# Performance work log

Hardware: AMD Instinct MI355X
Metric: run time of the kernel (lower is better)

The kernel has to match this reference:

```python
import jax, jax.numpy as jnp
import numpy as np

DIM, DIM_K, DIM_U, HEADS, SCOPE = 256, 16, 1, 4, 23
DIM_V = DIM // HEADS  # 64
EPS = 1e-5


def _bn(x, gamma, beta):
    # training-mode BatchNorm2d over (b, h, w), biased variance, per-channel affine
    mean = jnp.mean(x, axis=(0, 2, 3), keepdims=True)
    var = jnp.var(x, axis=(0, 2, 3), keepdims=True)
    xhat = (x - mean) * jax.lax.rsqrt(var + EPS)
    return xhat * gamma[None, :, None, None] + beta[None, :, None, None]


def setup_inputs() -> dict:
    key = jax.random.key(0)
    ks = jax.random.split(key, 8)
    c_out = HEADS * DIM_K + DIM_K * DIM_U + DIM_V * DIM_U  # 144
    x = jax.random.normal(ks[0], (16, DIM, 64, 64), dtype=jnp.float32)
    w_qkv = jax.random.normal(ks[1], (c_out, DIM), dtype=jnp.float32) * (1.0 / np.sqrt(DIM))
    gamma_q = jnp.ones((HEADS * DIM_K,), jnp.float32)
    beta_q = jnp.zeros((HEADS * DIM_K,), jnp.float32)
    gamma_v = jnp.ones((DIM_V * DIM_U,), jnp.float32)
    beta_v = jnp.zeros((DIM_V * DIM_U,), jnp.float32)
    fan_in = DIM_U * SCOPE * SCOPE
    w_lconv = jax.random.normal(ks[2], (DIM_K, DIM_U, 1, SCOPE, SCOPE), dtype=jnp.float32) * (1.0 / np.sqrt(fan_in))
    b_lconv = jnp.zeros((DIM_K,), jnp.float32)
    return {"x": x, "w_qkv": w_qkv, "gamma_q": gamma_q, "beta_q": beta_q,
            "gamma_v": gamma_v, "beta_v": beta_v, "w_lconv": w_lconv, "b_lconv": b_lconv}


def reference(x, w_qkv, gamma_q, beta_q, gamma_v, beta_v, w_lconv, b_lconv):
    b, c, h, w = x.shape
    m = h * w
    # 1x1 conv projection
    qkv = jnp.einsum('oc,bchw->bohw', w_qkv, x)
    q = qkv[:, :HEADS * DIM_K]
    k = qkv[:, HEADS * DIM_K:HEADS * DIM_K + DIM_K * DIM_U]
    v = qkv[:, HEADS * DIM_K + DIM_K * DIM_U:]
    # q: 'b (k n) h w -> b n k m'
    q = _bn(q, gamma_q, beta_q).reshape(b, DIM_K, HEADS, m).transpose(0, 2, 1, 3)
    # v: 'b (v u) h w -> b u v m'
    v = _bn(v, gamma_v, beta_v).reshape(b, DIM_V, DIM_U, m).transpose(0, 2, 1, 3)
    # k: 'b (u k) h w -> b u k m', softmax over m
    k = jax.nn.softmax(k.reshape(b, DIM_U, DIM_K, m), axis=-1)
    content_lambda = jnp.einsum('bukm,buvm->bkv', k, v)
    # position lambda: Conv3d over (v, h, w) with kernel (1, scope, scope)
    v5 = v.reshape(b, DIM_U, DIM_V, h, w)
    pad = (SCOPE - 1) // 2
    pl = jax.lax.conv_general_dilated(
        v5, w_lconv, window_strides=(1, 1, 1),
        padding=[(0, 0), (pad, pad), (pad, pad)],
        dimension_numbers=('NCDHW', 'OIDHW', 'NCDHW'))
    pl = pl + b_lconv[None, :, None, None, None]
    position_lambda = pl.reshape(b, DIM_K, DIM_V, m)
    content_output = jnp.einsum('bnkm,bkv->bnvm', q, content_lambda)
    position_output = jnp.einsum('bnkm,bkvm->bnvm', q, position_lambda)
    out = (content_output + position_output).reshape(b, HEADS * DIM_V, h, w)
    return out
```

## Files before the change

kernel.cpp:

```cpp
#include <hip/hip_runtime.h>
#include <math.h>

#define NB    16
#define CDIM  256
#define COUT  144
#define MPIX  4096
#define SCOPE 23
#define PADH  11
#define BNEPS 1e-5f

typedef __attribute__((ext_vector_type(4))) float f32x4;
typedef __attribute__((ext_vector_type(8))) short s16x8;

__device__ __forceinline__ unsigned short f2bf(float f) {
    unsigned u = __builtin_bit_cast(unsigned, f);
    unsigned r = (u + 0x7FFFu + ((u >> 16) & 1u)) >> 16;
    return (unsigned short)r;
}

__global__ void prep_frags(const float* __restrict__ w, const float* __restrict__ wl,
                           short* __restrict__ wqf, short* __restrict__ wfrag) {
    int i = blockIdx.x * 256 + threadIdx.x;
    if (i < 36864) {
        int j = i & 7, lane = (i >> 3) & 63;
        int fi = i >> 9;
        int mf = fi % 9, kc = fi / 9;
        int o = mf * 16 + (lane & 15);
        int c = kc * 32 + (lane >> 4) * 8 + j;
        wqf[i] = (short)f2bf(w[o * 256 + c]);
        return;
    }
    int i2 = i - 36864;
    if (i2 < 23 * 64 * 8) {
        int j = i2 & 7, l = (i2 >> 3) & 63, dy = i2 >> 9;
        int k = l & 15, t = ((l >> 4) << 3) + j;
        float wv = (t < SCOPE) ? wl[k * 529 + dy * 23 + t] : 0.f;
        wfrag[i2] = (short)f2bf(wv);
    }
}

__global__ void __launch_bounds__(256, 4) gemm_qkv(const float* __restrict__ x,
                                                   const short* __restrict__ wqf,
                                                   float* __restrict__ qkv) {
    __shared__ unsigned pk[16 * 65];
    int mt = blockIdx.x, b = blockIdx.y;
    int m0 = mt * 64;
    int tid = threadIdx.x;
    int px64 = tid & 63, c2b = tid >> 6;
    int lane = tid & 63, wv = tid >> 6;
    int pxl = lane & 15, kgq = lane >> 4;
    const float* xb = x + (size_t)b * CDIM * MPIX;
    float* qtb = qkv + (size_t)b * COUT * MPIX;
    const s16x8* wfv = (const s16x8*)wqf;

    f32x4 acc[9];
#pragma unroll
    for (int mf = 0; mf < 9; mf++) acc[mf] = 0.f;

#pragma unroll 1
    for (int kc = 0; kc < 8; kc++) {
        if (kc > 0) __syncthreads();
#pragma unroll
        for (int it = 0; it < 4; it++) {
            int c2 = c2b + it * 4;
            float x0 = xb[(size_t)(kc * 32 + 2 * c2) * MPIX + m0 + px64];
            float x1 = xb[(size_t)(kc * 32 + 2 * c2 + 1) * MPIX + m0 + px64];
            pk[c2 * 65 + px64] = (unsigned)f2bf(x0) | ((unsigned)f2bf(x1) << 16);
        }
        __syncthreads();
        const unsigned* bp = &pk[kgq * 4 * 65 + wv * 16 + pxl];
        int4 bi = make_int4(bp[0], bp[65], bp[130], bp[195]);
        s16x8 bf = __builtin_bit_cast(s16x8, bi);
#pragma unroll
        for (int mf = 0; mf < 9; mf++) {
            s16x8 af = wfv[(kc * 9 + mf) * 64 + lane];
            acc[mf] = __builtin_amdgcn_mfma_f32_16x16x32_bf16(af, bf, acc[mf], 0, 0, 0);
        }
    }

    int m = m0 + wv * 16 + pxl;
#pragma unroll
    for (int mf = 0; mf < 9; mf++) {
#pragma unroll
        for (int r = 0; r < 4; r++) {
            int o = mf * 16 + kgq * 4 + r;
            if (mf < 4) qtb[(size_t)m * 64 + o] = acc[mf][r];
            else qkv[((size_t)b * COUT + o) * MPIX + m] = acc[mf][r];
        }
    }
}

__global__ void stats_q(const float* __restrict__ qkv, float* __restrict__ qpart) {
    int mc = blockIdx.x, b = blockIdx.y;
    const float* qb = qkv + (size_t)b * COUT * MPIX;
    int tid = threadIdx.x;
    int c = tid & 63, mg = tid >> 6;
    float s = 0.f, s2 = 0.f;
#pragma unroll 4
    for (int i = 0; i < 64; i++) {
        int m = mc * 256 + i * 4 + mg;
        float v = qb[(size_t)m * 64 + c];
        s += v;
        s2 = fmaf(v, v, s2);
    }
    __shared__ float rs[4][64], rs2[4][64];
    rs[mg][c] = s;
    rs2[mg][c] = s2;
    __syncthreads();
    if (tid < 64) {
        float ts = rs[0][tid] + rs[1][tid] + rs[2][tid] + rs[3][tid];
        float ts2 = rs2[0][tid] + rs2[1][tid] + rs2[2][tid] + rs2[3][tid];
        qpart[(((size_t)tid * 16 + b) * 16 + mc) * 2 + 0] = ts;
        qpart[(((size_t)tid * 16 + b) * 16 + mc) * 2 + 1] = ts2;
    }
}

__global__ void stats_v(const float* __restrict__ qkv, float* __restrict__ part) {
    int cx = blockIdx.x, b = blockIdx.y;
    const float* row = qkv + ((size_t)b * COUT + 80 + cx) * MPIX;
    int tid = threadIdx.x;
    float s = 0.f, s2 = 0.f;
    for (int i = tid; i < MPIX; i += 256) {
        float v = row[i];
        s += v;
        s2 = fmaf(v, v, s2);
    }
#pragma unroll
    for (int off = 32; off > 0; off >>= 1) {
        s += __shfl_down(s, off);
        s2 += __shfl_down(s2, off);
    }
    __shared__ float red[8];
    int wid = tid >> 6, lane = tid & 63;
    if (lane == 0) { red[wid * 2] = s; red[wid * 2 + 1] = s2; }
    __syncthreads();
    if (tid == 0) {
        float ts = 0.f, ts2 = 0.f;
#pragma unroll
        for (int w2 = 0; w2 < 4; w2++) { ts += red[w2 * 2]; ts2 += red[w2 * 2 + 1]; }
        part[(size_t)((64 + cx) * 16 + b) * 2 + 0] = ts;
        part[(size_t)((64 + cx) * 16 + b) * 2 + 1] = ts2;
    }
}

__global__ void stats_finalize(const float* __restrict__ part,
                               const float* __restrict__ qpart,
                               const float* __restrict__ gq, const float* __restrict__ bq,
                               const float* __restrict__ gv, const float* __restrict__ bv,
                               float* __restrict__ ascale, float* __restrict__ dshift) {
    int ch = threadIdx.x;
    if (ch >= 128) return;
    float s = 0.f, s2 = 0.f;
    if (ch < 64) {
        for (int i = 0; i < 256; i++) {
            s += qpart[((size_t)ch * 256 + i) * 2 + 0];
            s2 += qpart[((size_t)ch * 256 + i) * 2 + 1];
        }
    } else {
        for (int b = 0; b < 16; b++) {
            s += part[(size_t)(ch * 16 + b) * 2 + 0];
            s2 += part[(size_t)(ch * 16 + b) * 2 + 1];
        }
    }
    const float invN = 1.0f / 65536.0f;
    float mean = s * invN;
    float var = s2 * invN - mean * mean;
    float g = (ch < 64) ? gq[ch] : gv[ch - 64];
    float be = (ch < 64) ? bq[ch] : bv[ch - 64];
    float a = g * rsqrtf(var + BNEPS);
    ascale[ch] = a;
    dshift[ch] = be - mean * a;
}

__global__ void softmax_k(const float* __restrict__ qkv, float* __restrict__ p) {
    int bk = blockIdx.x;
    int b = bk >> 4, kc = bk & 15;
    const float* row = qkv + ((size_t)b * COUT + 64 + kc) * MPIX;
    int tid = threadIdx.x;
    float v[16];
    float mx = -INFINITY;
#pragma unroll
    for (int i = 0; i < 16; i++) {
        v[i] = row[tid + i * 256];
        mx = fmaxf(mx, v[i]);
    }
#pragma unroll
    for (int off = 32; off > 0; off >>= 1) mx = fmaxf(mx, __shfl_down(mx, off));
    __shared__ float redm[4];
    __shared__ float bm;
    int wid = tid >> 6, lane = tid & 63;
    if (lane == 0) redm[wid] = mx;
    __syncthreads();
    if (tid == 0) bm = fmaxf(fmaxf(redm[0], redm[1]), fmaxf(redm[2], redm[3]));
    __syncthreads();
    mx = bm;
    float s = 0.f;
#pragma unroll
    for (int i = 0; i < 16; i++) {
        v[i] = expf(v[i] - mx);
        s += v[i];
    }
#pragma unroll
    for (int off = 32; off > 0; off >>= 1) s += __shfl_down(s, off);
    __shared__ float reds[4];
    __shared__ float bs;
    if (lane == 0) reds[wid] = s;
    __syncthreads();
    if (tid == 0) bs = reds[0] + reds[1] + reds[2] + reds[3];
    __syncthreads();
    float r = 1.0f / bs;
    float* prow = p + ((size_t)b * 16 + kc) * MPIX;
#pragma unroll
    for (int i = 0; i < 16; i++) prow[tid + i * 256] = v[i] * r;
}

__global__ void cl_partial(const float* __restrict__ qkv, const float* __restrict__ p,
                           const float* __restrict__ ascale, const float* __restrict__ dshift,
                           float* __restrict__ clpart) {
    __shared__ float vsT[128][65];
    int mc = blockIdx.x, b = blockIdx.y;
    int m0 = mc * 256;
    int tid = threadIdx.x;
    int vc = tid & 63, kg = tid >> 6;
    float acc[4] = {0.f, 0.f, 0.f, 0.f};
    for (int half = 0; half < 2; half++) {
        int mh = m0 + half * 128;
        __syncthreads();
        for (int i = tid; i < 64 * 128; i += 256) {
            int r = i >> 7, c = i & 127;
            vsT[c][r] = fmaf(ascale[64 + r], qkv[((size_t)b * COUT + 80 + r) * MPIX + mh + c],
                             dshift[64 + r]);
        }
        __syncthreads();
        for (int mm = 0; mm < 128; mm++) {
            float vv = vsT[mm][vc];
#pragma unroll
            for (int i = 0; i < 4; i++) {
                int kc = kg * 4 + i;
                acc[i] = fmaf(p[((size_t)b * 16 + kc) * MPIX + mh + mm], vv, acc[i]);
            }
        }
    }
#pragma unroll
    for (int i = 0; i < 4; i++) {
        int kc = kg * 4 + i;
        clpart[(((size_t)b * 16 + mc) * 16 + kc) * 64 + vc] = acc[i];
    }
}

__global__ void cl_reduce(const float* __restrict__ clpart, float* __restrict__ cl) {
    int b = blockIdx.x;
    for (int o = threadIdx.x; o < 1024; o += 256) {
        float s = 0.f;
        for (int mc = 0; mc < 16; mc++)
            s += clpart[((size_t)b * 16 + mc) * 1024 + o];
        cl[(size_t)b * 1024 + o] = s;
    }
}

__global__ void __launch_bounds__(256) bnq_t(float* __restrict__ qkv,
                                             const float* __restrict__ ascale,
                                             const float* __restrict__ dshift) {
    __shared__ float sv[64][65];
    int mt = blockIdx.x, b = blockIdx.y;
    int m0 = mt * 64;
    float* qb = qkv + (size_t)b * COUT * MPIX;
    int tid = threadIdx.x;
    int c = tid & 63, mg = tid >> 6;
    float a = ascale[c], d = dshift[c];
#pragma unroll
    for (int i = 0; i < 16; i++) {
        int m = mg * 16 + i;
        sv[m][c] = fmaf(a, qb[(size_t)(m0 + m) * 64 + c], d);
    }
    __syncthreads();
    int m = tid >> 2, jb = (tid & 3) * 8;
    unsigned dw[8];
#pragma unroll
    for (int j = 0; j < 8; j++) {
        int cc = jb * 2 + 2 * j;
        dw[j] = (unsigned)f2bf(sv[m][cc]) | ((unsigned)f2bf(sv[m][cc + 1]) << 16);
    }
    unsigned* dst = (unsigned*)qb + (size_t)(m0 + m) * 64 + jb;
    *(uint4*)dst = make_uint4(dw[0], dw[1], dw[2], dw[3]);
    *(uint4*)(dst + 4) = make_uint4(dw[4], dw[5], dw[6], dw[7]);
}

#define SPW 88
#define LD_FRAG(P) __builtin_bit_cast(s16x8, make_int4((P)[0], (P)[2], (P)[4], (P)[6]))
#define STEP(DY, J) do {                                                        \
    const unsigned* pnew_ = xbase + ((DY) + 3) * SPW;                           \
    rw[((J) + 3) & 3][0] = LD_FRAG(pnew_);                                      \
    rw[((J) + 3) & 3][1] = LD_FRAG(pnew_ + 16);                                 \
    int dyn_ = ((DY) + 3 < 22) ? (DY) + 3 : 22;                                 \
    wr[((J) + 3) & 3] = wf[dyn_ * 64 + lane];                                   \
    _Pragma("unroll")                                                           \
    for (int ty_ = 0; ty_ < 4; ty_++) {                                         \
      _Pragma("unroll")                                                         \
      for (int x2_ = 0; x2_ < 2; x2_++) {                                       \
        int t_ = ty_ * 2 + x2_;                                                 \
        acc[t_] = __builtin_amdgcn_mfma_f32_16x16x32_bf16(                      \
            wr[(J) & 3], rw[((J) + ty_) & 3][x2_], acc[t_], 0, 0, 0);           \
      }                                                                         \
    }                                                                           \
  } while (0)

__global__ void __launch_bounds__(256, 4) lambda_main(
    const float* __restrict__ qkv, const float* __restrict__ ascale,
    const float* __restrict__ dshift, const float* __restrict__ cl,
    const short* __restrict__ wfrag, const float* __restrict__ bl,
    float* __restrict__ out) {
    __shared__ unsigned spack[54 * SPW + 8];
    __shared__ float sck[16];

    int vc = blockIdx.x, b = blockIdx.y, h = blockIdx.z;
    int tid = threadIdx.x;

    if (tid < 16) sck[tid] = cl[((size_t)b * 16 + tid) * 64 + vc] + bl[tid];

    float av = ascale[64 + vc], dv = dshift[64 + vc];
    const float* vrow = qkv + ((size_t)b * COUT + 80 + vc) * MPIX;
    for (int i = tid; i < 54 * SPW; i += 256) {
        int y = i / SPW, e = i - y * SPW;
        int iy = h * 32 + y - PADH;
        float f0 = 0.f, f1 = 0.f;
        if ((unsigned)iy < 64u) {
            int ix0 = e - PADH, ix1 = e - PADH + 1;
            if ((unsigned)ix0 < 64u) f0 = fmaf(av, vrow[iy * 64 + ix0], dv);
            if ((unsigned)ix1 < 64u) f1 = fmaf(av, vrow[iy * 64 + ix1], dv);
        }
        spack[i] = (unsigned)f2bf(f0) | ((unsigned)f2bf(f1) << 16);
    }
    if (tid < 8) spack[54 * SPW + tid] = 0u;
    __syncthreads();

    int lane = tid & 63;
    int wv = tid >> 6;
    int px = lane & 15;
    int kg = lane >> 4;
    const s16x8* wf = (const s16x8*)wfrag;

    const unsigned* qtb = (const unsigned*)(qkv + (size_t)b * COUT * MPIX);
    float* ob = out + (size_t)b * 256 * MPIX;

    float sck_l[4];
#pragma unroll
    for (int r = 0; r < 4; r++) sck_l[r] = sck[kg * 4 + r];

#pragma unroll 1
    for (int gg = 0; gg < 2; gg++) {
        int y0 = (gg * 4 + wv) * 4;
        const unsigned* base = &spack[y0 * SPW + px + kg * 8];

#pragma unroll 1
        for (int xh = 0; xh < 2; xh++) {
            const unsigned* xbase = base + xh * 32;
            f32x4 acc[8];
#pragma unroll
            for (int t = 0; t < 8; t++) acc[t] = 0.f;

            s16x8 rw[4][2];
            s16x8 wr[4];
#pragma unroll
            for (int r0 = 0; r0 < 3; r0++) {
                const unsigned* p = xbase + r0 * SPW;
                rw[r0][0] = LD_FRAG(p);
                rw[r0][1] = LD_FRAG(p + 16);
            }
#pragma unroll
            for (int s = 0; s < 3; s++) wr[s] = wf[s * 64 + lane];

#pragma unroll 1
            for (int i8 = 0; i8 < 2; i8++) {
                int dyb = i8 * 8;
                STEP(dyb + 0, 0);
                STEP(dyb + 1, 1);
                STEP(dyb + 2, 2);
                STEP(dyb + 3, 3);
                STEP(dyb + 4, 4);
                STEP(dyb + 5, 5);
                STEP(dyb + 6, 6);
                STEP(dyb + 7, 7);
            }
            STEP(16, 0);
            STEP(17, 1);
            STEP(18, 2);
            STEP(19, 3);
            STEP(20, 4);
            STEP(21, 5);
            STEP(22, 6);

#pragma unroll
            for (int t = 0; t < 8; t++) {
                int ty = t >> 1, x2 = t & 1;
                int m0 = (h * 32 + y0 + ty) * 64 + (xh * 2 + x2) * 16;
                float lam[4];
#pragma unroll
                for (int r = 0; r < 4; r++) lam[r] = acc[t][r] + sck_l[r];
                const unsigned* qp = &qtb[(size_t)(m0 + px) * 64 + kg * 8];
                uint4 qa = *(const uint4*)qp;
                uint4 qb4 = *(const uint4*)(qp + 4);
                unsigned dws[8] = {qa.x, qa.y, qa.z, qa.w, qb4.x, qb4.y, qb4.z, qb4.w};
                float po[4] = {0.f, 0.f, 0.f, 0.f};
#pragma unroll
                for (int d = 0; d < 8; d++) {
                    float q0 = __builtin_bit_cast(float, dws[d] << 16);
                    float q1 = __builtin_bit_cast(float, dws[d] & 0xffff0000u);
                    int i0 = 2 * d, i1 = 2 * d + 1;
                    po[i0 & 3] = fmaf(q0, lam[i0 >> 2], po[i0 & 3]);
                    po[i1 & 3] = fmaf(q1, lam[i1 >> 2], po[i1 & 3]);
                }
#pragma unroll
                for (int n = 0; n < 4; n++) {
                    po[n] += __shfl_xor(po[n], 16);
                    po[n] += __shfl_xor(po[n], 32);
                }
                float sv = (kg == 0) ? po[0] : (kg == 1) ? po[1] : (kg == 2) ? po[2] : po[3];
                ob[(size_t)(kg * 64 + vc) * MPIX + m0 + px] = sv;
            }
        }
    }
}

extern "C" void kernel_launch(void* const* d_in, const int* in_sizes, int n_in,
                              void* d_out, int out_size, void* d_ws, size_t ws_size,
                              hipStream_t stream) {
    const float* x      = (const float*)d_in[0];
    const float* w_qkv  = (const float*)d_in[1];
    const float* gq     = (const float*)d_in[2];
    const float* bq     = (const float*)d_in[3];
    const float* gv     = (const float*)d_in[4];
    const float* bv     = (const float*)d_in[5];
    const float* wl     = (const float*)d_in[6];
    const float* bl     = (const float*)d_in[7];
    float* out = (float*)d_out;

    float* ws     = (float*)d_ws;
    float* qkv    = ws;
    float* p      = qkv + 9437184;
    float* part   = p + 1048576;
    float* ascale = part + 4096;
    float* dshift = ascale + 128;
    float* clpart = dshift + 128;
    float* clb    = clpart + 262144;
    short* wfrag  = (short*)(clb + 16384);
    short* wqf    = (short*)(clb + 16384 + 5888 + 64);
    float* qpart  = (float*)(wqf + 36864);

    prep_frags<<<190, 256, 0, stream>>>(w_qkv, wl, wqf, wfrag);
    gemm_qkv<<<dim3(64, 16), 256, 0, stream>>>(x, wqf, qkv);
    stats_q<<<dim3(16, 16), 256, 0, stream>>>(qkv, qpart);
    stats_v<<<dim3(64, 16), 256, 0, stream>>>(qkv, part);
    stats_finalize<<<1, 128, 0, stream>>>(part, qpart, gq, bq, gv, bv, ascale, dshift);
    softmax_k<<<256, 256, 0, stream>>>(qkv, p);
    cl_partial<<<dim3(16, 16), 256, 0, stream>>>(qkv, p, ascale, dshift, clpart);
    cl_reduce<<<16, 256, 0, stream>>>(clpart, clb);
    bnq_t<<<dim3(64, 16), 256, 0, stream>>>(qkv, ascale, dshift);
    lambda_main<<<dim3(64, 16, 2), 256, 0, stream>>>(qkv, ascale, dshift, clb, wfrag, bl, out);
}
```

Baseline: 208.7 us.

## Fuse BatchNorm channel statistics into QKV GEMM epilogue

Computes per-channel sum and sum-of-squares of the projection output inside the GEMM epilogue, using lane shuffles and a shared-memory reduction across waves. This replaces the separate stats_q and stats_v kernels, which reread the q and v regions of the qkv buffer from global memory. The finalize kernel becomes a 128-block parallel reduction over 1024 partials per channel. In exchange the GEMM gains extra shuffles, shared memory and a barrier, which may reduce its occupancy, and it also computes statistics for the unused k channels.

```diff
diff --git a/kernel.cpp b/kernel.cpp
--- a/kernel.cpp
+++ b/kernel.cpp
@@ -41,8 +41,10 @@
 
 __global__ void __launch_bounds__(256, 4) gemm_qkv(const float* __restrict__ x,
                                                    const short* __restrict__ wqf,
-                                                   float* __restrict__ qkv) {
+                                                   float* __restrict__ qkv,
+                                                   float* __restrict__ statpart) {
     __shared__ unsigned pk[16 * 65];
+    __shared__ float ssum[4][144], ssq[4][144];
     int mt = blockIdx.x, b = blockIdx.y;
     int m0 = mt * 64;
     int tid = threadIdx.x;
@@ -88,42 +90,47 @@
             else qkv[((size_t)b * COUT + o) * MPIX + m] = acc[mf][r];
         }
     }
-}
-
-__global__ void stats_q(const float* __restrict__ qkv, float* __restrict__ qpart) {
-    int mc = blockIdx.x, b = blockIdx.y;
-    const float* qb = qkv + (size_t)b * COUT * MPIX;
-    int tid = threadIdx.x;
-    int c = tid & 63, mg = tid >> 6;
+
+#pragma unroll
+    for (int mf = 0; mf < 9; mf++) {
+#pragma unroll
+        for (int r = 0; r < 4; r++) {
+            float s = acc[mf][r];
+            float s2 = s * s;
+#pragma unroll
+            for (int off = 1; off < 16; off <<= 1) {
+                s += __shfl_xor(s, off);
+                s2 += __shfl_xor(s2, off);
+            }
+            if (pxl == 0) {
+                int ch = mf * 16 + kgq * 4 + r;
+                ssum[wv][ch] = s;
+                ssq[wv][ch] = s2;
+            }
+        }
+    }
+    __syncthreads();
+    if (tid < 144) {
+        float s = ssum[0][tid] + ssum[1][tid] + ssum[2][tid] + ssum[3][tid];
+        float s2 = ssq[0][tid] + ssq[1][tid] + ssq[2][tid] + ssq[3][tid];
+        size_t idx = (((size_t)tid * 16 + b) * 64 + mt) * 2;
+        statpart[idx + 0] = s;
+        statpart[idx + 1] = s2;
+    }
+}
+
+__global__ void stats_finalize(const float* __restrict__ statpart,
+                               const float* __restrict__ gq, const float* __restrict__ bq,
+                               const float* __restrict__ gv, const float* __restrict__ bv,
+                               float* __restrict__ ascale, float* __restrict__ dshift) {
+    int sch = blockIdx.x;
+    int gch = (sch < 64) ? sch : sch + 16;
+    const float* sp = statpart + (size_t)gch * 1024 * 2;
+    int tid = threadIdx.x;
     float s = 0.f, s2 = 0.f;
-#pragma unroll 4
-    for (int i = 0; i < 64; i++) {
-        int m = mc * 256 + i * 4 + mg;
-        float v = qb[(size_t)m * 64 + c];
-        s += v;
-        s2 = fmaf(v, v, s2);
-    }
-    __shared__ float rs[4][64], rs2[4][64];
-    rs[mg][c] = s;
-    rs2[mg][c] = s2;
-    __syncthreads();
-    if (tid < 64) {
-        float ts = rs[0][tid] + rs[1][tid] + rs[2][tid] + rs[3][tid];
-        float ts2 = rs2[0][tid] + rs2[1][tid] + rs2[2][tid] + rs2[3][tid];
-        qpart[(((size_t)tid * 16 + b) * 16 + mc) * 2 + 0] = ts;
-        qpart[(((size_t)tid * 16 + b) * 16 + mc) * 2 + 1] = ts2;
-    }
-}
-
-__global__ void stats_v(const float* __restrict__ qkv, float* __restrict__ part) {
-    int cx = blockIdx.x, b = blockIdx.y;
-    const float* row = qkv + ((size_t)b * COUT + 80 + cx) * MPIX;
-    int tid = threadIdx.x;
-    float s = 0.f, s2 = 0.f;
-    for (int i = tid; i < MPIX; i += 256) {
-        float v = row[i];
-        s += v;
-        s2 = fmaf(v, v, s2);
+    for (int i = tid; i < 1024; i += 256) {
+        s += sp[i * 2 + 0];
+        s2 += sp[i * 2 + 1];
     }
 #pragma unroll
     for (int off = 32; off > 0; off >>= 1) {
@@ -138,38 +145,15 @@
         float ts = 0.f, ts2 = 0.f;
 #pragma unroll
         for (int w2 = 0; w2 < 4; w2++) { ts += red[w2 * 2]; ts2 += red[w2 * 2 + 1]; }
-        part[(size_t)((64 + cx) * 16 + b) * 2 + 0] = ts;
-        part[(size_t)((64 + cx) * 16 + b) * 2 + 1] = ts2;
-    }
-}
-
-__global__ void stats_finalize(const float* __restrict__ part,
-                               const float* __restrict__ qpart,
-                               const float* __restrict__ gq, const float* __restrict__ bq,
-                               const float* __restrict__ gv, const float* __restrict__ bv,
-                               float* __restrict__ ascale, float* __restrict__ dshift) {
-    int ch = threadIdx.x;
-    if (ch >= 128) return;
-    float s = 0.f, s2 = 0.f;
-    if (ch < 64) {
-        for (int i = 0; i < 256; i++) {
-            s += qpart[((size_t)ch * 256 + i) * 2 + 0];
-            s2 += qpart[((size_t)ch * 256 + i) * 2 + 1];
-        }
-    } else {
-        for (int b = 0; b < 16; b++) {
-            s += part[(size_t)(ch * 16 + b) * 2 + 0];
-            s2 += part[(size_t)(ch * 16 + b) * 2 + 1];
-        }
-    }
-    const float invN = 1.0f / 65536.0f;
-    float mean = s * invN;
-    float var = s2 * invN - mean * mean;
-    float g = (ch < 64) ? gq[ch] : gv[ch - 64];
-    float be = (ch < 64) ? bq[ch] : bv[ch - 64];
-    float a = g * rsqrtf(var + BNEPS);
-    ascale[ch] = a;
-    dshift[ch] = be - mean * a;
+        const float invN = 1.0f / 65536.0f;
+        float mean = ts * invN;
+        float var = ts2 * invN - mean * mean;
+        float g = (sch < 64) ? gq[sch] : gv[sch - 64];
+        float be = (sch < 64) ? bq[sch] : bv[sch - 64];
+        float a = g * rsqrtf(var + BNEPS);
+        ascale[sch] = a;
+        dshift[sch] = be - mean * a;
+    }
 }
 
 __global__ void softmax_k(const float* __restrict__ qkv, float* __restrict__ p) {
@@ -438,20 +422,17 @@
     float* ws     = (float*)d_ws;
     float* qkv    = ws;
     float* p      = qkv + 9437184;
-    float* part   = p + 1048576;
-    float* ascale = part + 4096;
+    float* ascale = p + 1048576;
     float* dshift = ascale + 128;
     float* clpart = dshift + 128;
     float* clb    = clpart + 262144;
     short* wfrag  = (short*)(clb + 16384);
     short* wqf    = (short*)(clb + 16384 + 5888 + 64);
-    float* qpart  = (float*)(wqf + 36864);
+    float* statpart = (float*)(wqf + 36864);
 
     prep_frags<<<190, 256, 0, stream>>>(w_qkv, wl, wqf, wfrag);
-    gemm_qkv<<<dim3(64, 16), 256, 0, stream>>>(x, wqf, qkv);
-    stats_q<<<dim3(16, 16), 256, 0, stream>>>(qkv, qpart);
-    stats_v<<<dim3(64, 16), 256, 0, stream>>>(qkv, part);
-    stats_finalize<<<1, 128, 0, stream>>>(part, qpart, gq, bq, gv, bv, ascale, dshift);
+    gemm_qkv<<<dim3(64, 16), 256, 0, stream>>>(x, wqf, qkv, statpart);
+    stats_finalize<<<128, 256, 0, stream>>>(statpart, gq, bq, gv, bv, ascale, dshift);
     softmax_k<<<256, 256, 0, stream>>>(qkv, p);
     cl_partial<<<dim3(16, 16), 256, 0, stream>>>(qkv, p, ascale, dshift, clpart);
     cl_reduce<<<16, 256, 0, stream>>>(clpart, clb);
```

New measurement: 202.1 us. 1.03x faster.
